# Optimization experiments

Hardware: AMD Instinct MI355X
Metric: run time of the kernel (lower is better)

The kernel has to match this reference:

```python
import jax, jax.numpy as jnp
import numpy as np


def _knn_idx(query, ref, k):
    # query [B,Q,F], ref [B,M,F] -> indices [B,Q,k] of k nearest refs (L2)
    d2 = (jnp.sum(query * query, -1)[..., None]
          - 2.0 * jnp.einsum('bqf,bmf->bqm', query, ref)
          + jnp.sum(ref * ref, -1)[:, None, :])
    _, idx = jax.lax.top_k(-d2, k)
    return idx


def _gather(pts, idx):
    # pts [B,M,F], idx [B,Q,k] -> [B,Q,k,F]
    return jax.vmap(lambda p, i: p[i])(pts, idx)


def _mlp(h, W1, b1, W2, b2):
    # pointwise 1x1-conv MLP: Conv1d(k=1) == per-point matmul
    return jax.nn.relu(h @ W1 + b1) @ W2 + b2


def setup_inputs() -> dict:
    key = jax.random.key(0)
    ks = jax.random.split(key, 12)
    B, N, S1, S2 = 8, 16384, 512, 128

    def p(k, shape, fan):
        return jax.random.normal(k, shape, jnp.float32) / np.float32(np.sqrt(fan))

    return {
        'x': jax.random.normal(ks[0], (B, N, 3), jnp.float32),
        'sample_idx1': jnp.sort(jax.random.randint(ks[1], (S1,), 0, N)),
        'sample_idx2': jnp.sort(jax.random.randint(ks[2], (S2,), 0, S1)),
        'sa1_W1': p(ks[3], (3, 64), 3), 'sa1_b1': jnp.zeros((64,), jnp.float32),
        'sa1_W2': p(ks[4], (64, 64), 64), 'sa1_b2': jnp.zeros((64,), jnp.float32),
        'sa2_W1': p(ks[5], (64, 128), 64), 'sa2_b1': jnp.zeros((128,), jnp.float32),
        'sa2_W2': p(ks[6], (128, 128), 128), 'sa2_b2': jnp.zeros((128,), jnp.float32),
        'fp1_W1': p(ks[7], (192, 64), 192), 'fp1_b1': jnp.zeros((64,), jnp.float32),
        'fp1_W2': p(ks[8], (64, 64), 64), 'fp1_b2': jnp.zeros((64,), jnp.float32),
        'fp2_W1': p(ks[9], (67, 32), 67), 'fp2_b1': jnp.zeros((32,), jnp.float32),
        'fp2_W2': p(ks[10], (32, 32), 32), 'fp2_b2': jnp.zeros((32,), jnp.float32),
        'fc_W': p(ks[11], (32, 2), 32), 'fc_b': jnp.zeros((2,), jnp.float32),
    }


def reference(x, sample_idx1, sample_idx2,
              sa1_W1, sa1_b1, sa1_W2, sa1_b2,
              sa2_W1, sa2_b1, sa2_W2, sa2_b2,
              fp1_W1, fp1_b1, fp1_W2, fp1_b2,
              fp2_W1, fp2_b1, fp2_W2, fp2_b2,
              fc_W, fc_b):
    G = 32  # group_points
    # --- SetAbstraction 1 (KNN grouping in xyz space) ---
    samp1 = x[:, sample_idx1]                                  # [B,S1,3]
    g1 = _gather(x, _knn_idx(samp1, x, G))                     # [B,S1,G,3]
    feat1 = jnp.max(_mlp(g1, sa1_W1, sa1_b1, sa1_W2, sa1_b2), axis=2)   # [B,S1,64]
    # --- SetAbstraction 2 (point cloud = SA1 features, as in source) ---
    samp2 = feat1[:, sample_idx2]                              # [B,S2,64]
    g2 = _gather(feat1, _knn_idx(samp2, feat1, G))             # [B,S2,G,64]
    feat2 = jnp.max(_mlp(g2, sa2_W1, sa2_b1, sa2_W2, sa2_b2), axis=2)   # [B,S2,128]
    coords2 = samp1[:, sample_idx2]                            # [B,S2,3]
    # --- FeaturePropagation 1: interpolate feat2 onto the S1 points (3-NN mean) ---
    interp1 = jnp.mean(_gather(feat2, _knn_idx(samp1, coords2, 3)), axis=2)  # [B,S1,128]
    h1 = _mlp(jnp.concatenate([feat1, interp1], -1), fp1_W1, fp1_b1, fp1_W2, fp1_b2)  # [B,S1,64]
    # --- FeaturePropagation 2: interpolate onto all N points ---
    interp2 = jnp.mean(_gather(h1, _knn_idx(x, samp1, 3)), axis=2)           # [B,N,64]
    h2 = _mlp(jnp.concatenate([x, interp2], -1), fp2_W1, fp2_b1, fp2_W2, fp2_b2)      # [B,N,32]
    return jax.nn.sigmoid(h2 @ fc_W + fc_b)                    # [B,N,2]
```

## Files before the change

kernel.cpp:

```cpp
#include <hip/hip_runtime.h>
#include <hip/hip_bf16.h>

#define NB   8
#define NPTS 16384
#define NS1  512
#define NS2  128
#define KNN  32
#define FINF 3.402823466e+38f

__device__ __forceinline__ unsigned sortkey(float f) {
  unsigned u = __float_as_uint(f);
  unsigned m = (u & 0x80000000u) ? 0xFFFFFFFFu : 0x80000000u;
  return u ^ m;
}

__device__ __forceinline__ void topk32_u32(unsigned key, int idx, int lane,
                                           unsigned& lkey, int& lidx,
                                           unsigned& tau) {
  const bool is16 = (lane == 16);
  unsigned long long mask = __ballot(key < tau);
  while (mask) {
    const int src = (int)(__ffsll((long long)mask) - 1);
    mask &= mask - 1;
    const unsigned ck = (unsigned)__builtin_amdgcn_readlane((int)key, src);
    if (ck < tau) {
      const int ci = __builtin_amdgcn_readlane(idx, src);
      const int upk0 = __builtin_amdgcn_update_dpp(0, (int)lkey, 0x111, 0xf, 0xf, true);
      const int upi0 = __builtin_amdgcn_update_dpp(0, lidx, 0x111, 0xf, 0xf, true);
      const int pk = __builtin_amdgcn_readlane((int)lkey, 15);
      const int pi = __builtin_amdgcn_readlane(lidx, 15);
      const unsigned up  = is16 ? (unsigned)pk : (unsigned)upk0;
      const int     upi  = is16 ? pi : upi0;
      const bool keep  = (lkey <= ck);
      const bool useup = (up > ck);
      const unsigned nk = keep ? lkey : (useup ? up : ck);
      const int     ni  = keep ? lidx : (useup ? upi : ci);
      if (lane < 32) { lkey = nk; lidx = ni; }
      tau = (unsigned)__builtin_amdgcn_readlane((int)lkey, 31);
    }
  }
}

__device__ __forceinline__ void merge3(float& d0, int& j0, float& d1, int& j1,
                                       float& d2, int& j2, int xm) {
  float e0 = __shfl_xor(d0, xm), e1 = __shfl_xor(d1, xm), e2 = __shfl_xor(d2, xm);
  int   f0 = __shfl_xor(j0, xm), f1 = __shfl_xor(j1, xm), f2 = __shfl_xor(j2, xm);
  float a0 = d0, a1 = d1, a2 = d2;
  int   b0 = j0, b1 = j1, b2 = j2;
  float od0, od1, od2; int oj0, oj1, oj2;
  #pragma unroll
  for (int r = 0; r < 3; ++r) {
    bool ta = (a0 < e0) || (a0 == e0 && b0 < f0);
    float sd = ta ? a0 : e0; int sj = ta ? b0 : f0;
    a0 = ta ? a1 : a0;  b0 = ta ? b1 : b0;
    a1 = ta ? a2 : a1;  b1 = ta ? b2 : b1;
    a2 = ta ? FINF : a2;
    e0 = ta ? e0 : e1;  f0 = ta ? f0 : f1;
    e1 = ta ? e1 : e2;  f1 = ta ? f1 : f2;
    e2 = ta ? e2 : FINF;
    if (r == 0) { od0 = sd; oj0 = sj; }
    else if (r == 1) { od1 = sd; oj1 = sj; }
    else { od2 = sd; oj2 = sj; }
  }
  d0 = od0; j0 = oj0; d1 = od1; j1 = oj1; d2 = od2; j2 = oj2;
}

extern "C" __global__ void __launch_bounds__(256)
prep_kernel(const float* __restrict__ x, float4* __restrict__ xr) {
  const int i = blockIdx.x * 256 + threadIdx.x;
  const float rx = x[i*3+0], ry = x[i*3+1], rz = x[i*3+2];
  xr[i] = make_float4(rx, ry, rz, rx*rx + ry*ry + rz*rz);
}

#define PROC32(rr, jbase)                                                     \
  {                                                                           \
    const float d = (Q.w - 2.0f*(Q.x*rr.x + Q.y*rr.y + Q.z*rr.z)) + rr.w;     \
    topk32_u32(sortkey(d), (jbase) + lane, lane, lkey, lidx, tau);            \
  }

extern "C" __global__ void __launch_bounds__(256, 8)
knn1_kernel(const float4* __restrict__ xr, const int* __restrict__ sidx1,
            int* __restrict__ idx1) {
  __shared__ unsigned SK[2][32];
  __shared__ int      SI[2][32];
  const int w = threadIdx.x >> 6, lane = threadIdx.x & 63;
  const int lq = w >> 1, half = w & 1;
  const int gq = blockIdx.x * 2 + lq;
  const int b = gq >> 9, q = gq & (NS1 - 1);
  const float4* xb = xr + (size_t)b * NPTS;
  const float4 Q = xb[sidx1[q]];
  const float4* xw = xb + half * (NPTS/2);
  const int jb0 = half * (NPTS/2);
  unsigned lkey = 0xFFFFFFFFu, tau = 0xFFFFFFFFu;
  int lidx = 0;
  float4 r0 = xw[0*64+lane], r1 = xw[1*64+lane], r2 = xw[2*64+lane], r3 = xw[3*64+lane];
  float4 r4 = xw[4*64+lane], r5 = xw[5*64+lane], r6 = xw[6*64+lane], r7 = xw[7*64+lane];
  for (int t = 0; t < 128; t += 8) {
    PROC32(r0, jb0 + (t+0)*64);  r0 = xw[((t+ 8)&127)*64 + lane];
    PROC32(r1, jb0 + (t+1)*64);  r1 = xw[((t+ 9)&127)*64 + lane];
    PROC32(r2, jb0 + (t+2)*64);  r2 = xw[((t+10)&127)*64 + lane];
    PROC32(r3, jb0 + (t+3)*64);  r3 = xw[((t+11)&127)*64 + lane];
    PROC32(r4, jb0 + (t+4)*64);  r4 = xw[((t+12)&127)*64 + lane];
    PROC32(r5, jb0 + (t+5)*64);  r5 = xw[((t+13)&127)*64 + lane];
    PROC32(r6, jb0 + (t+6)*64);  r6 = xw[((t+14)&127)*64 + lane];
    PROC32(r7, jb0 + (t+7)*64);  r7 = xw[((t+15)&127)*64 + lane];
  }
  if (half == 1 && lane < 32) { SK[lq][lane] = lkey; SI[lq][lane] = lidx; }
  __syncthreads();
  if (half == 0) {
    const unsigned mk = (lane < 32) ? SK[lq][lane] : 0xFFFFFFFFu;
    const int      mi = (lane < 32) ? SI[lq][lane] : 0;
    topk32_u32(mk, mi, lane, lkey, lidx, tau);
    if (lane < 32) idx1[gq*KNN + lane] = lidx;
  }
}

extern "C" __global__ void __launch_bounds__(256)
mlp1_kernel(const float* __restrict__ x, const int* __restrict__ sidx1,
            const int* __restrict__ idx1,
            const float* __restrict__ W1, const float* __restrict__ b1,
            const float* __restrict__ W2, const float* __restrict__ b2,
            float* __restrict__ feat1, float* __restrict__ rr1,
            float* __restrict__ samp1) {
  __shared__ float P[32][3];
  __shared__ float H[32][64];
  __shared__ float PM[4][64];
  const int tid = threadIdx.x;
  const int gq = blockIdx.x;
  const int b = gq >> 9, q = gq & (NS1-1);
  const float* xb = x + (size_t)b * NPTS * 3;
  const int* nb = idx1 + gq * KNN;
  if (tid < 96) { int n = tid/3, d = tid - n*3; P[n][d] = xb[nb[n]*3 + d]; }
  __syncthreads();
  #pragma unroll
  for (int i = 0; i < 8; ++i) {
    int e = tid + 256*i, n = e >> 6, c = e & 63;
    float h = b1[c] + P[n][0]*W1[c] + P[n][1]*W1[64+c] + P[n][2]*W1[128+c];
    H[n][c] = fmaxf(h, 0.0f);
  }
  __syncthreads();
  const int g = tid >> 6, c = tid & 63;
  float acc[8];
  #pragma unroll
  for (int k = 0; k < 8; ++k) acc[k] = 0.0f;
  for (int j = 0; j < 64; j += 4) {
    float w0 = W2[j*64+c], w1 = W2[(j+1)*64+c], w2 = W2[(j+2)*64+c], w3 = W2[(j+3)*64+c];
    #pragma unroll
    for (int k = 0; k < 8; ++k) {
      float4 h4 = *(const float4*)&H[g*8+k][j];
      acc[k] = fmaf(h4.w, w3, fmaf(h4.z, w2, fmaf(h4.y, w1, fmaf(h4.x, w0, acc[k]))));
    }
  }
  float m = acc[0];
  #pragma unroll
  for (int k = 1; k < 8; ++k) m = fmaxf(m, acc[k]);
  PM[g][c] = m;
  __syncthreads();
  if (tid < 64) {
    float v = fmaxf(fmaxf(PM[0][tid], PM[1][tid]), fmaxf(PM[2][tid], PM[3][tid])) + b2[tid];
    feat1[(size_t)gq*64 + tid] = v;
    float s = v*v;
    #pragma unroll
    for (int off = 32; off; off >>= 1) s += __shfl_xor(s, off);
    if (tid == 0) rr1[gq] = s;
  } else if (tid < 67) {
    int d = tid - 64;
    samp1[(size_t)gq*3 + d] = xb[sidx1[q]*3 + d];
  }
}

extern "C" __global__ void __launch_bounds__(256)
knn2_kernel(const float* __restrict__ feat1, const float* __restrict__ rr1,
            const int* __restrict__ sidx2, int* __restrict__ idx2) {
  __shared__ float qrow[4][64];
  const int w = threadIdx.x >> 6, lane = threadIdx.x & 63;
  const int gq = blockIdx.x*4 + w;
  const int b = gq >> 7, q = gq & (NS2-1);
  const int sq = sidx2[q];
  const float* f1b = feat1 + (size_t)b * NS1 * 64;
  const float* rrb = rr1 + b * NS1;
  qrow[w][lane] = f1b[sq*64 + lane];
  __syncthreads();
  const float qq = rrb[sq];
  unsigned lkey = 0xFFFFFFFFu, tau = 0xFFFFFFFFu;
  int lidx = 0;
  for (int t = 0; t < NS1/64; ++t) {
    const int j = t*64 + lane;
    const float* rrow = f1b + j*64;
    float dot = 0.0f;
    #pragma unroll
    for (int f = 0; f < 64; f += 4) {
      float4 r4 = *(const float4*)(rrow + f);
      dot = fmaf(qrow[w][f+3], r4.w, fmaf(qrow[w][f+2], r4.z,
            fmaf(qrow[w][f+1], r4.y, fmaf(qrow[w][f+0], r4.x, dot))));
    }
    const float d = (qq - 2.0f*dot) + rrb[j];
    topk32_u32(sortkey(d), j, lane, lkey, lidx, tau);
  }
  if (lane < 32) idx2[gq*KNN + lane] = lidx;
}

extern "C" __global__ void __launch_bounds__(256)
mlp2_kernel(const float* __restrict__ feat1, const int* __restrict__ idx2,
            const float* __restrict__ W1, const float* __restrict__ b1,
            const float* __restrict__ W2, const float* __restrict__ b2,
            float* __restrict__ feat2) {
  __shared__ float Gm[32][64];
  __shared__ float H[32][128];
  __shared__ float PM[2][128];
  const int tid = threadIdx.x;
  const int gq = blockIdx.x;
  const int b = gq >> 7;
  const float* f1b = feat1 + (size_t)b * NS1 * 64;
  const int* nb = idx2 + gq * KNN;
  #pragma unroll
  for (int i = 0; i < 8; ++i) {
    int e = tid + 256*i, n = e >> 6, f = e & 63;
    Gm[n][f] = f1b[nb[n]*64 + f];
  }
  __syncthreads();
  #pragma unroll
  for (int i = 0; i < 16; ++i) {
    int e = tid + 256*i, n = e >> 7, c = e & 127;
    float h = b1[c];
    for (int f = 0; f < 64; f += 4) {
      float4 g4 = *(const float4*)&Gm[n][f];
      h = fmaf(g4.x, W1[f*128+c], h);
      h = fmaf(g4.y, W1[(f+1)*128+c], h);
      h = fmaf(g4.z, W1[(f+2)*128+c], h);
      h = fmaf(g4.w, W1[(f+3)*128+c], h);
    }
    H[n][c] = fmaxf(h, 0.0f);
  }
  __syncthreads();
  const int g = tid >> 7, c = tid & 127;
  float acc[16];
  #pragma unroll
  for (int k = 0; k < 16; ++k) acc[k] = 0.0f;
  for (int j = 0; j < 128; j += 4) {
    float w0 = W2[j*128+c], w1 = W2[(j+1)*128+c], w2 = W2[(j+2)*128+c], w3 = W2[(j+3)*128+c];
    #pragma unroll
    for (int k = 0; k < 16; ++k) {
      float4 h4 = *(const float4*)&H[g*16+k][j];
      acc[k] = fmaf(h4.w, w3, fmaf(h4.z, w2, fmaf(h4.y, w1, fmaf(h4.x, w0, acc[k]))));
    }
  }
  float m = acc[0];
  #pragma unroll
  for (int k = 1; k < 16; ++k) m = fmaxf(m, acc[k]);
  PM[g][c] = m;
  __syncthreads();
  if (tid < 128) feat2[(size_t)gq*128 + tid] = fmaxf(PM[0][tid], PM[1][tid]) + b2[tid];
}

extern "C" __global__ void __launch_bounds__(256)
fp1_kernel(const float* __restrict__ samp1, const int* __restrict__ sidx2,
           const float* __restrict__ feat1, const float* __restrict__ feat2,
           const float* __restrict__ W1, const float* __restrict__ b1,
           const float* __restrict__ W2, const float* __restrict__ b2,
           float* __restrict__ h1) {
  __shared__ float interp[4][128];
  __shared__ float hbuf[4][64];
  const int w = threadIdx.x >> 6, lane = threadIdx.x & 63;
  const int gq = blockIdx.x*4 + w;
  const int b = gq >> 9, q = gq & (NS1-1);
  const float* s1b = samp1 + (size_t)b * NS1 * 3;
  const float qx = s1b[q*3+0], qy = s1b[q*3+1], qz = s1b[q*3+2];
  const float qq = qx*qx + qy*qy + qz*qz;
  float d0, d1; int j0i, j1i;
  {
    const int rs = sidx2[lane];
    const float rx = s1b[rs*3+0], ry = s1b[rs*3+1], rz = s1b[rs*3+2];
    d0 = (qq - 2.0f*(qx*rx+qy*ry+qz*rz)) + (rx*rx+ry*ry+rz*rz);
    j0i = lane;
  }
  {
    const int j = lane + 64;
    const int rs = sidx2[j];
    const float rx = s1b[rs*3+0], ry = s1b[rs*3+1], rz = s1b[rs*3+2];
    d1 = (qq - 2.0f*(qx*rx+qy*ry+qz*rz)) + (rx*rx+ry*ry+rz*rz);
    j1i = j;
  }
  if (d1 < d0) { float td = d0; d0 = d1; d1 = td; int tj = j0i; j0i = j1i; j1i = tj; }
  float dA = d0, dB = d1, dC = FINF;
  int   jA = j0i, jB = j1i, jC = 0;
  merge3(dA, jA, dB, jB, dC, jC, 1);
  merge3(dA, jA, dB, jB, dC, jC, 2);
  merge3(dA, jA, dB, jB, dC, jC, 4);
  merge3(dA, jA, dB, jB, dC, jC, 8);
  merge3(dA, jA, dB, jB, dC, jC, 16);
  merge3(dA, jA, dB, jB, dC, jC, 32);
  const int r0 = jA, r1 = jB, r2 = jC;
  const float* f2b = feat2 + (size_t)b * NS2 * 128;
  interp[w][lane] =
      (f2b[r0*128+lane] + f2b[r1*128+lane] + f2b[r2*128+lane]) * (1.0f/3.0f);
  interp[w][lane+64] =
      (f2b[r0*128+64+lane] + f2b[r1*128+64+lane] + f2b[r2*128+64+lane]) * (1.0f/3.0f);
  __syncthreads();
  const float* f1row = feat1 + (size_t)gq * 64;
  float h = b1[lane];
  for (int f = 0; f < 64; ++f)  h = fmaf(f1row[f], W1[f*64+lane], h);
  for (int f = 0; f < 128; ++f) h = fmaf(interp[w][f], W1[(64+f)*64+lane], h);
  hbuf[w][lane] = fmaxf(h, 0.0f);
  __syncthreads();
  float o = b2[lane];
  for (int f = 0; f < 64; ++f) o = fmaf(hbuf[w][f], W2[f*64+lane], o);
  h1[(size_t)gq*64 + lane] = o;
}

extern "C" __global__ void __launch_bounds__(256, 4)
fp2a_kernel(const float* __restrict__ x, const float* __restrict__ samp1,
            ushort4* __restrict__ knn3) {
  __shared__ float4 RS[NS1];
  const int tid = threadIdx.x;
  const int b = blockIdx.x >> 8;
  const int pbase = (blockIdx.x & 255) * 64;
  for (int e = tid; e < NS1; e += 256) {
    const float rx = samp1[((size_t)b*NS1 + e)*3 + 0];
    const float ry = samp1[((size_t)b*NS1 + e)*3 + 1];
    const float rz = samp1[((size_t)b*NS1 + e)*3 + 2];
    RS[e] = make_float4(rx, ry, rz, rx*rx + ry*ry + rz*rz);
  }
  __syncthreads();
  const int p = pbase + (tid >> 2);
  const int q4 = tid & 3;
  const float* xb = x + (size_t)b * NPTS * 3;
  const float qx = xb[p*3+0], qy = xb[p*3+1], qz = xb[p*3+2];
  const float qq = qx*qx + qy*qy + qz*qz;
  float d0 = FINF, d1 = FINF, d2 = FINF;
  int j0 = 0, j1 = 0, j2 = 0;
  const float4* RQ = RS + q4*128;
  #pragma unroll 4
  for (int i = 0; i < 128; ++i) {
    const float4 r = RQ[i];
    const float dot = qx*r.x + qy*r.y + qz*r.z;
    const float d = (qq - 2.0f*dot) + r.w;
    const int j = q4*128 + i;
    const bool c2 = d < d2, c1 = d < d1, c0 = d < d0;
    d2 = c1 ? d1 : (c2 ? d : d2);  j2 = c1 ? j1 : (c2 ? j : j2);
    d1 = c0 ? d0 : (c1 ? d : d1);  j1 = c0 ? j0 : (c1 ? j : j1);
    d0 = c0 ? d : d0;              j0 = c0 ? j : j0;
  }
  merge3(d0, j0, d1, j1, d2, j2, 1);
  merge3(d0, j0, d1, j1, d2, j2, 2);
  if (q4 == 0) {
    ushort4 o;
    o.x = (unsigned short)j0; o.y = (unsigned short)j1;
    o.z = (unsigned short)j2; o.w = 0;
    knn3[(size_t)b*NPTS + p] = o;
  }
}

extern "C" __global__ void __launch_bounds__(256, 4)
fp2b_kernel(const float* __restrict__ x, const ushort4* __restrict__ knn3,
            const float* __restrict__ h1,
            const float* __restrict__ W1, const float* __restrict__ b1,
            const float* __restrict__ W2, const float* __restrict__ b2,
            const float* __restrict__ fcW, const float* __restrict__ fcb,
            float* __restrict__ out) {
  __shared__ float Xe[64][68];
  __shared__ float W1s[67*32];
  __shared__ float Hs[64][36];
  __shared__ ushort4 kid[64];
  __shared__ float WcS[64];
  __shared__ float bcS[2];
  const int tid = threadIdx.x;
  const int b = blockIdx.x >> 8;
  const int pbase = (blockIdx.x & 255) * 64;
  const float* xb = x + (size_t)b * NPTS * 3;
  const float* h1b = h1 + (size_t)b * NS1 * 64;
  if (tid < 64) {
    kid[tid] = knn3[(size_t)b*NPTS + pbase + tid];
    Xe[tid][0] = xb[(pbase+tid)*3+0];
    Xe[tid][1] = xb[(pbase+tid)*3+1];
    Xe[tid][2] = xb[(pbase+tid)*3+2];
  }
  for (int e = tid; e < 67*32; e += 256) W1s[e] = W1[e];
  __syncthreads();
  {
    const int sub = tid >> 6, f = tid & 63;
    #pragma unroll 4
    for (int i = 0; i < 16; ++i) {
      const int p = i*4 + sub;
      const ushort4 kk = kid[p];
      const float v = (h1b[(int)kk.x*64 + f] + h1b[(int)kk.y*64 + f] +
                       h1b[(int)kk.z*64 + f]) * (1.0f/3.0f);
      Xe[p][3+f] = v;
    }
  }
  __syncthreads();
  if (tid < 64) {
    const int k = tid >> 1, col = tid & 1;
    float s = 0.0f;
    for (int c = 0; c < 32; ++c) s = fmaf(W2[k*32+c], fcW[c*2+col], s);
    WcS[k*2+col] = s;
  } else if (tid < 66) {
    const int col = tid & 1;
    float s = fcb[col];
    for (int c = 0; c < 32; ++c) s = fmaf(b2[c], fcW[c*2+col], s);
    bcS[col] = s;
  }
  {
    const int p = tid >> 2, c0 = (tid & 3) * 8;
    float acc[8];
    const float4 bb0 = *(const float4*)(b1 + c0);
    const float4 bb1 = *(const float4*)(b1 + c0 + 4);
    acc[0]=bb0.x; acc[1]=bb0.y; acc[2]=bb0.z; acc[3]=bb0.w;
    acc[4]=bb1.x; acc[5]=bb1.y; acc[6]=bb1.z; acc[7]=bb1.w;
    for (int f = 0; f < 67; ++f) {
      const float xv = Xe[p][f];
      const float4 w0 = *(const float4*)&W1s[f*32 + c0];
      const float4 w1 = *(const float4*)&W1s[f*32 + c0 + 4];
      acc[0] = fmaf(xv, w0.x, acc[0]);
      acc[1] = fmaf(xv, w0.y, acc[1]);
      acc[2] = fmaf(xv, w0.z, acc[2]);
      acc[3] = fmaf(xv, w0.w, acc[3]);
      acc[4] = fmaf(xv, w1.x, acc[4]);
      acc[5] = fmaf(xv, w1.y, acc[5]);
      acc[6] = fmaf(xv, w1.z, acc[6]);
      acc[7] = fmaf(xv, w1.w, acc[7]);
    }
    *(float4*)&Hs[p][c0]   = make_float4(fmaxf(acc[0],0.f), fmaxf(acc[1],0.f),
                                         fmaxf(acc[2],0.f), fmaxf(acc[3],0.f));
    *(float4*)&Hs[p][c0+4] = make_float4(fmaxf(acc[4],0.f), fmaxf(acc[5],0.f),
                                         fmaxf(acc[6],0.f), fmaxf(acc[7],0.f));
  }
  __syncthreads();
  if (tid < 128) {
    const int p = tid >> 1, col = tid & 1;
    float s = bcS[col];
    for (int c = 0; c < 32; ++c) s = fmaf(Hs[p][c], WcS[c*2+col], s);
    out[((size_t)b*NPTS + pbase + p)*2 + col] = 1.0f / (1.0f + expf(-s));
  }
}

extern "C" void kernel_launch(void* const* d_in, const int* in_sizes, int n_in,
                              void* d_out, int out_size, void* d_ws, size_t ws_size,
                              hipStream_t stream) {
  const float* x     = (const float*)d_in[0];
  const int*   sidx1 = (const int*)d_in[1];
  const int*   sidx2 = (const int*)d_in[2];
  const float* sa1W1 = (const float*)d_in[3];
  const float* sa1b1 = (const float*)d_in[4];
  const float* sa1W2 = (const float*)d_in[5];
  const float* sa1b2 = (const float*)d_in[6];
  const float* sa2W1 = (const float*)d_in[7];
  const float* sa2b1 = (const float*)d_in[8];
  const float* sa2W2 = (const float*)d_in[9];
  const float* sa2b2 = (const float*)d_in[10];
  const float* fp1W1 = (const float*)d_in[11];
  const float* fp1b1 = (const float*)d_in[12];
  const float* fp1W2 = (const float*)d_in[13];
  const float* fp1b2 = (const float*)d_in[14];
  const float* fp2W1 = (const float*)d_in[15];
  const float* fp2b1 = (const float*)d_in[16];
  const float* fp2W2 = (const float*)d_in[17];
  const float* fp2b2 = (const float*)d_in[18];
  const float* fcW   = (const float*)d_in[19];
  const float* fcb   = (const float*)d_in[20];
  float* out = (float*)d_out;

  char* ws = (char*)d_ws;
  float4* xr   = (float4*)(ws + 0);
  float* feat1 = (float*)(ws + 0);
  float* rr1   = (float*)(ws + 1048576);
  float* samp1 = (float*)(ws + 1064960);
  float* feat2 = (float*)(ws + 1114112);
  float* h1    = (float*)(ws + 1638400);
  int*   idx1  = (int*)  (ws + 2686976);
  int*   idx2  = (int*)  (ws + 3211264);
  ushort4* knn3 = (ushort4*)(ws + 0);

  hipLaunchKernelGGL(prep_kernel, dim3(512), dim3(256), 0, stream, x, xr);
  hipLaunchKernelGGL(knn1_kernel, dim3(2048), dim3(256), 0, stream,
                     xr, sidx1, idx1);
  hipLaunchKernelGGL(mlp1_kernel, dim3(4096), dim3(256), 0, stream,
                     x, sidx1, idx1, sa1W1, sa1b1, sa1W2, sa1b2,
                     feat1, rr1, samp1);
  hipLaunchKernelGGL(knn2_kernel, dim3(256), dim3(256), 0, stream,
                     feat1, rr1, sidx2, idx2);
  hipLaunchKernelGGL(mlp2_kernel, dim3(1024), dim3(256), 0, stream,
                     feat1, idx2, sa2W1, sa2b1, sa2W2, sa2b2, feat2);
  hipLaunchKernelGGL(fp1_kernel, dim3(1024), dim3(256), 0, stream,
                     samp1, sidx2, feat1, feat2, fp1W1, fp1b1, fp1W2, fp1b2, h1);
  hipLaunchKernelGGL(fp2a_kernel, dim3(2048), dim3(256), 0, stream,
                     x, samp1, knn3);
  hipLaunchKernelGGL(fp2b_kernel, dim3(2048), dim3(256), 0, stream,
                     x, knn3, h1, fp2W1, fp2b1, fp2W2, fp2b2, fcW, fcb, out);
}
```

Measured before the change: 273.4 us.

## Share pruning threshold between KNN half-waves and use float keys directly

```diff
diff --git a/kernel.cpp b/kernel.cpp
--- a/kernel.cpp
+++ b/kernel.cpp
@@ -7,36 +7,33 @@
 #define NS2  128
 #define KNN  32
 #define FINF 3.402823466e+38f
-
-__device__ __forceinline__ unsigned sortkey(float f) {
-  unsigned u = __float_as_uint(f);
-  unsigned m = (u & 0x80000000u) ? 0xFFFFFFFFu : 0x80000000u;
-  return u ^ m;
-}
-
-__device__ __forceinline__ void topk32_u32(unsigned key, int idx, int lane,
-                                           unsigned& lkey, int& lidx,
-                                           unsigned& tau) {
+#define NINF_BITS ((int)0xFF800000)
+
+__device__ __forceinline__ void topk32f(float key, int idx, int lane,
+                                        float& lkey, int& lidx, float& tau,
+                                        unsigned long long mask) {
   const bool is16 = (lane == 16);
-  unsigned long long mask = __ballot(key < tau);
   while (mask) {
     const int src = (int)(__ffsll((long long)mask) - 1);
     mask &= mask - 1;
-    const unsigned ck = (unsigned)__builtin_amdgcn_readlane((int)key, src);
+    const float ck = __int_as_float(
+        __builtin_amdgcn_readlane(__float_as_int(key), src));
     if (ck < tau) {
       const int ci = __builtin_amdgcn_readlane(idx, src);
-      const int upk0 = __builtin_amdgcn_update_dpp(0, (int)lkey, 0x111, 0xf, 0xf, true);
-      const int upi0 = __builtin_amdgcn_update_dpp(0, lidx, 0x111, 0xf, 0xf, true);
-      const int pk = __builtin_amdgcn_readlane((int)lkey, 15);
+      const int upk0 = __builtin_amdgcn_update_dpp(
+          NINF_BITS, __float_as_int(lkey), 0x111, 0xf, 0xf, false);
+      const int upi0 = __builtin_amdgcn_update_dpp(
+          0, lidx, 0x111, 0xf, 0xf, false);
+      const int pk = __builtin_amdgcn_readlane(__float_as_int(lkey), 15);
       const int pi = __builtin_amdgcn_readlane(lidx, 15);
-      const unsigned up  = is16 ? (unsigned)pk : (unsigned)upk0;
-      const int     upi  = is16 ? pi : upi0;
+      const float up  = __int_as_float(is16 ? pk : upk0);
+      const int   upi = is16 ? pi : upi0;
       const bool keep  = (lkey <= ck);
       const bool useup = (up > ck);
-      const unsigned nk = keep ? lkey : (useup ? up : ck);
-      const int     ni  = keep ? lidx : (useup ? upi : ci);
+      const float nk = keep ? lkey : (useup ? up : ck);
+      const int   ni = keep ? lidx : (useup ? upi : ci);
       if (lane < 32) { lkey = nk; lidx = ni; }
-      tau = (unsigned)__builtin_amdgcn_readlane((int)lkey, 31);
+      tau = __int_as_float(__builtin_amdgcn_readlane(__float_as_int(lkey), 31));
     }
   }
 }
@@ -72,45 +69,56 @@
   xr[i] = make_float4(rx, ry, rz, rx*rx + ry*ry + rz*rz);
 }
 
-#define PROC32(rr, jbase)                                                     \
+#define PROCF(rr, jbase)                                                      \
   {                                                                           \
+    const float tp = *tauP_p;                                                 \
     const float d = (Q.w - 2.0f*(Q.x*rr.x + Q.y*rr.y + Q.z*rr.z)) + rr.w;     \
-    topk32_u32(sortkey(d), (jbase) + lane, lane, lkey, lidx, tau);            \
+    const unsigned long long mask = __ballot(d < tau && d <= tp);             \
+    if (mask) {                                                               \
+      topk32f(d, (jbase) + lane, lane, lkey, lidx, tau, mask);                \
+      if (lane == 0) *tauO_p = tau;                                           \
+    }                                                                         \
   }
 
 extern "C" __global__ void __launch_bounds__(256, 8)
 knn1_kernel(const float4* __restrict__ xr, const int* __restrict__ sidx1,
             int* __restrict__ idx1) {
-  __shared__ unsigned SK[2][32];
-  __shared__ int      SI[2][32];
+  __shared__ float SK[2][32];
+  __shared__ int   SI[2][32];
+  __shared__ float TAUS[2][2];
   const int w = threadIdx.x >> 6, lane = threadIdx.x & 63;
   const int lq = w >> 1, half = w & 1;
   const int gq = blockIdx.x * 2 + lq;
   const int b = gq >> 9, q = gq & (NS1 - 1);
   const float4* xb = xr + (size_t)b * NPTS;
   const float4 Q = xb[sidx1[q]];
+  if (lane == 0) TAUS[lq][half] = FINF;
+  __syncthreads();
+  volatile float* tauP_p = &TAUS[lq][half ^ 1];
+  volatile float* tauO_p = &TAUS[lq][half];
   const float4* xw = xb + half * (NPTS/2);
   const int jb0 = half * (NPTS/2);
-  unsigned lkey = 0xFFFFFFFFu, tau = 0xFFFFFFFFu;
+  float lkey = FINF, tau = FINF;
   int lidx = 0;
   float4 r0 = xw[0*64+lane], r1 = xw[1*64+lane], r2 = xw[2*64+lane], r3 = xw[3*64+lane];
   float4 r4 = xw[4*64+lane], r5 = xw[5*64+lane], r6 = xw[6*64+lane], r7 = xw[7*64+lane];
   for (int t = 0; t < 128; t += 8) {
-    PROC32(r0, jb0 + (t+0)*64);  r0 = xw[((t+ 8)&127)*64 + lane];
-    PROC32(r1, jb0 + (t+1)*64);  r1 = xw[((t+ 9)&127)*64 + lane];
-    PROC32(r2, jb0 + (t+2)*64);  r2 = xw[((t+10)&127)*64 + lane];
-    PROC32(r3, jb0 + (t+3)*64);  r3 = xw[((t+11)&127)*64 + lane];
-    PROC32(r4, jb0 + (t+4)*64);  r4 = xw[((t+12)&127)*64 + lane];
-    PROC32(r5, jb0 + (t+5)*64);  r5 = xw[((t+13)&127)*64 + lane];
-    PROC32(r6, jb0 + (t+6)*64);  r6 = xw[((t+14)&127)*64 + lane];
-    PROC32(r7, jb0 + (t+7)*64);  r7 = xw[((t+15)&127)*64 + lane];
+    PROCF(r0, jb0 + (t+0)*64);  r0 = xw[((t+ 8)&127)*64 + lane];
+    PROCF(r1, jb0 + (t+1)*64);  r1 = xw[((t+ 9)&127)*64 + lane];
+    PROCF(r2, jb0 + (t+2)*64);  r2 = xw[((t+10)&127)*64 + lane];
+    PROCF(r3, jb0 + (t+3)*64);  r3 = xw[((t+11)&127)*64 + lane];
+    PROCF(r4, jb0 + (t+4)*64);  r4 = xw[((t+12)&127)*64 + lane];
+    PROCF(r5, jb0 + (t+5)*64);  r5 = xw[((t+13)&127)*64 + lane];
+    PROCF(r6, jb0 + (t+6)*64);  r6 = xw[((t+14)&127)*64 + lane];
+    PROCF(r7, jb0 + (t+7)*64);  r7 = xw[((t+15)&127)*64 + lane];
   }
   if (half == 1 && lane < 32) { SK[lq][lane] = lkey; SI[lq][lane] = lidx; }
   __syncthreads();
   if (half == 0) {
-    const unsigned mk = (lane < 32) ? SK[lq][lane] : 0xFFFFFFFFu;
-    const int      mi = (lane < 32) ? SI[lq][lane] : 0;
-    topk32_u32(mk, mi, lane, lkey, lidx, tau);
+    const float mk = (lane < 32) ? SK[lq][lane] : FINF;
+    const int   mi = (lane < 32) ? SI[lq][lane] : 0;
+    const unsigned long long mmask = __ballot(mk < tau);
+    topk32f(mk, mi, lane, lkey, lidx, tau, mmask);
     if (lane < 32) idx1[gq*KNN + lane] = lidx;
   }
 }
@@ -182,7 +190,7 @@
   qrow[w][lane] = f1b[sq*64 + lane];
   __syncthreads();
   const float qq = rrb[sq];
-  unsigned lkey = 0xFFFFFFFFu, tau = 0xFFFFFFFFu;
+  float lkey = FINF, tau = FINF;
   int lidx = 0;
   for (int t = 0; t < NS1/64; ++t) {
     const int j = t*64 + lane;
@@ -195,7 +203,8 @@
             fmaf(qrow[w][f+1], r4.y, fmaf(qrow[w][f+0], r4.x, dot))));
     }
     const float d = (qq - 2.0f*dot) + rrb[j];
-    topk32_u32(sortkey(d), j, lane, lkey, lidx, tau);
+    const unsigned long long mask = __ballot(d < tau);
+    if (mask) topk32f(d, j, lane, lkey, lidx, tau, mask);
   }
   if (lane < 32) idx2[gq*KNN + lane] = lidx;
 }
```

After: 312.7 us. +14.4%, slower.
